# Kernel tuning notes

Hardware: AMD Instinct MI355X
Metric: run time of the kernel (lower is better)

Reference implementation:

```python
import jax, jax.numpy as jnp
import numpy as np

KCODES = 8  # kcodes from init


def setup_inputs() -> dict:
    key = jax.random.key(0)
    k1, k2 = jax.random.split(key)
    x = jax.random.normal(k1, (4, 2048, 768), dtype=jnp.float32)          # [B, S, D]
    codebook = jax.random.normal(k2, (8192, 768), dtype=jnp.float32)      # [N, D] embedding weight
    return {"x": x, "codebook": codebook}


def reference(x, codebook):
    # EuclideanSnapFunction.forward with default hook_kwargs
    # (keep_k_codes=True, no disabled codes/tokens):
    #   logits = -cdist(x, codebook, p=2); topk(kcodes); gather; mean over k.
    # Top-k over -dist is identical to top-k over -dist^2, so we use squared
    x2 = jnp.sum(x * x, axis=-1, keepdims=True)                 # [B, S, 1]
    c2 = jnp.sum(codebook * codebook, axis=-1)                  # [N]
    xc = jnp.einsum('bsd,nd->bsn', x, codebook)                 # [B, S, N]
    neg_d2 = 2.0 * xc - x2 - c2                                 # -squared dist
    _, codebook_ids = jax.lax.top_k(neg_d2, KCODES)             # [B, S, K]
    quant = codebook[codebook_ids]                              # [B, S, K, D] gather
    outputs = quant.sum(axis=-2) / KCODES                       # masked averaging over k codes
    return outputs, codebook_ids
```

## Files before the change

### kernel.cpp

```cpp
#include <hip/hip_runtime.h>

#define T_TOK 8192
#define DIM   768
#define NCB   8192
#define KSEL  8
#define BT    64
#define BN    128
#define BD    32
#define NQ    (BD/4)
#define CSTR  9
#define DSTR  140

typedef float v2f __attribute__((ext_vector_type(2)));

__global__ __launch_bounds__(256) void sq_pairwise_kernel(
    const float* __restrict__ cb, const float* __restrict__ x,
    float* __restrict__ c2out, float* __restrict__ x2out)
{
  #pragma clang fp contract(off)
  __shared__ float part[32][8];
  const int tid = threadIdx.x;
  const int row = blockIdx.x * 32 + (tid >> 3);
  const int b   = tid & 7;
  const float* src = (row < NCB) ? (cb + (size_t)row * DIM)
                                 : (x + (size_t)(row - NCB) * DIM);
  const float* a = src + 96 * b;

  float s[16];
  #pragma unroll
  for (int l = 0; l < 16; ++l) {
    float v, t;
    v = a[l];       t = v * v; float r0 = t;
    v = a[64 + l];  t = v * v; r0 = r0 + t;
    v = a[80 + l];  t = v * v; r0 = r0 + t;
    v = a[16 + l];  t = v * v; float r1 = t;
    v = a[32 + l];  t = v * v; float r2 = t;
    v = a[48 + l];  t = v * v; float r3 = t;
    s[l] = (r0 + r1) + (r2 + r3);
  }
  float t1[8], t2[4];
  #pragma unroll
  for (int i = 0; i < 8; ++i) t1[i] = s[i] + s[i + 8];
  #pragma unroll
  for (int j = 0; j < 4; ++j) t2[j] = t1[j] + t1[j + 4];
  part[tid >> 3][b] = (t2[0] + t2[2]) + (t2[1] + t2[3]);
  __syncthreads();

  if (b == 0) {
    const float* p = part[tid >> 3];
    float res = ((p[0] + p[1]) + (p[2] + p[3])) + ((p[4] + p[5]) + (p[6] + p[7]));
    if (row < NCB) c2out[row] = res;
    else           x2out[row - NCB] = res;
  }
}

__global__ __launch_bounds__(256, 2) void dist_topk_kernel(
    const float* __restrict__ x, const float* __restrict__ cb,
    const float* __restrict__ c2g, const float* __restrict__ x2g,
    float* __restrict__ ws, int ncodes)
{
  #pragma clang fp contract(off)
  __shared__ float4 smem4[2240];
  float*  smem = (float*)smem4;
  float4* xs4  = smem4;
  float4* cs4  = smem4 + NQ * BT;

  const int tid  = threadIdx.x;
  const int t0   = blockIdx.x * BT;
  const int nbeg = blockIdx.y * ncodes;

  const int gx = tid & 15;
  const int gy = tid >> 4;

  const int tt = tid >> 2;
  const int cc = tid & 3;

  const int xr  = tid >> 2;
  const int xq  = tid & 3;
  const int cr  = tid >> 1;
  const int cq0 = (tid & 1) * 4;
  const int crg = (cr >> 3) * CSTR + (cr & 7);

  float x2r[4];
  #pragma unroll
  for (int i = 0; i < 4; ++i) x2r[i] = x2g[t0 + gy * 4 + i];

  float bdist[KSEL]; int bid[KSEL];
  #pragma unroll
  for (int i = 0; i < KSEL; ++i) { bdist[i] = __builtin_inff(); bid[i] = 0x7fffffff; }
  float bmax = __builtin_inff(); int bmaxid = 0x7fffffff; int bslot = 0;

  for (int n0 = nbeg; n0 < nbeg + ncodes; n0 += BN) {
    float c2r[8];
    #pragma unroll
    for (int j = 0; j < 8; ++j) c2r[j] = c2g[n0 + gx * 8 + j];

    v2f accL[4][8], accH[4][8];
    #pragma unroll
    for (int i = 0; i < 4; ++i)
      #pragma unroll
      for (int j = 0; j < 8; ++j) { accL[i][j] = (v2f)0.f; accH[i][j] = (v2f)0.f; }

    float4 xpre0, xpre1, cpre0, cpre1, cpre2, cpre3;
    {
      const float* xp = x + (size_t)(t0 + xr) * DIM + xq * 4;
      xpre0 = *(const float4*)xp;
      xpre1 = *(const float4*)(xp + 16);
      const float* cp = cb + (size_t)(n0 + cr) * DIM + cq0 * 4;
      cpre0 = *(const float4*)(cp + 0);
      cpre1 = *(const float4*)(cp + 4);
      cpre2 = *(const float4*)(cp + 8);
      cpre3 = *(const float4*)(cp + 12);
    }

    for (int d0 = 0; d0 < DIM; d0 += BD) {
      __syncthreads();
      xs4[xq * BT + xr]       = xpre0;
      xs4[(xq + 4) * BT + xr] = xpre1;
      cs4[(cq0 + 0) * 16 * CSTR + crg] = cpre0;
      cs4[(cq0 + 1) * 16 * CSTR + crg] = cpre1;
      cs4[(cq0 + 2) * 16 * CSTR + crg] = cpre2;
      cs4[(cq0 + 3) * 16 * CSTR + crg] = cpre3;
      __syncthreads();

      const int dn = d0 + BD;
      if (dn < DIM) {
        const float* xp = x + (size_t)(t0 + xr) * DIM + dn + xq * 4;
        xpre0 = *(const float4*)xp;
        xpre1 = *(const float4*)(xp + 16);
        const float* cp = cb + (size_t)(n0 + cr) * DIM + dn + cq0 * 4;
        cpre0 = *(const float4*)(cp + 0);
        cpre1 = *(const float4*)(cp + 4);
        cpre2 = *(const float4*)(cp + 8);
        cpre3 = *(const float4*)(cp + 12);
      }

      #pragma unroll
      for (int q = 0; q < NQ; ++q) {
        float4 xa[4];
        #pragma unroll
        for (int i = 0; i < 4; ++i) xa[i] = xs4[q * BT + gy * 4 + i];
        #pragma unroll
        for (int j = 0; j < 8; ++j) {
          const float4 cv = cs4[q * 16 * CSTR + gx * CSTR + j];
          #pragma unroll
          for (int i = 0; i < 4; ++i) {
            v2f a, b, p;
            a[0] = xa[i].x; a[1] = xa[i].y;
            b[0] = cv.x;    b[1] = cv.y;
            p = a * b;
            accL[i][j] = accL[i][j] + p;
            a[0] = xa[i].z; a[1] = xa[i].w;
            b[0] = cv.z;    b[1] = cv.w;
            p = a * b;
            accH[i][j] = accH[i][j] + p;
          }
        }
      }
    }

    __syncthreads();
    #pragma unroll
    for (int i = 0; i < 4; ++i) {
      float v[8];
      #pragma unroll
      for (int j = 0; j < 8; ++j) {
        float xc = (accL[i][j][0] + accH[i][j][0]) + (accL[i][j][1] + accH[i][j][1]);
        float s  = 2.0f * xc - x2r[i];
        v[j] = -(s - c2r[j]);
      }
      float4* dp = (float4*)&smem[(gy * 4 + i) * DSTR + gx * 8];
      dp[0] = make_float4(v[0], v[1], v[2], v[3]);
      dp[1] = make_float4(v[4], v[5], v[6], v[7]);
    }
    __syncthreads();

    #pragma unroll
    for (int i2 = 0; i2 < BN / 4; ++i2) {
      const float dval = smem[tt * DSTR + cc + 4 * i2];
      const int   id   = n0 + cc + 4 * i2;
      if (dval < bmax) {
        #pragma unroll
        for (int q = 0; q < KSEL; ++q)
          if (q == bslot) { bdist[q] = dval; bid[q] = id; }
        bmax = bdist[0]; bmaxid = bid[0]; bslot = 0;
        #pragma unroll
        for (int q = 1; q < KSEL; ++q)
          if (bdist[q] > bmax || (bdist[q] == bmax && bid[q] > bmaxid)) {
            bmax = bdist[q]; bmaxid = bid[q]; bslot = q;
          }
      }
    }
  }

  __syncthreads();
  float* md = smem;
  int*   mi = (int*)smem + 2048;
  #pragma unroll
  for (int j = 0; j < KSEL; ++j) {
    md[tt * 32 + cc * KSEL + j] = bdist[j];
    mi[tt * 32 + cc * KSEL + j] = bid[j];
  }
  __syncthreads();
  if (tid < BT) {
    float* mdt = md + tid * 32;
    int*   mit = mi + tid * 32;
    const size_t base = ((size_t)blockIdx.y * T_TOK + (t0 + tid)) * 16;
    for (int r = 0; r < KSEL; ++r) {
      float best = __builtin_inff(); int bestid = 0x7fffffff; int bs = 0;
      for (int s = 0; s < 32; ++s) {
        const float dv = mdt[s]; const int iv = mit[s];
        if (dv < best || (dv == best && iv < bestid)) { best = dv; bestid = iv; bs = s; }
      }
      mdt[bs] = __builtin_inff();
      ws[base + r] = best;
      ((int*)ws)[base + 8 + r] = bestid;
    }
  }
}

__global__ __launch_bounds__(192) void merge_gather_kernel(
    const float* __restrict__ cb, const float* __restrict__ ws,
    float* __restrict__ out, float* __restrict__ out_ids, int nsplit)
{
  __shared__ float mv[64];
  __shared__ int   mid[64];
  __shared__ int   ssel[KSEL];

  const int t   = blockIdx.x;
  const int tid = threadIdx.x;
  const int ncand = nsplit * KSEL;

  if (tid < ncand) {
    const int s = tid >> 3, r = tid & 7;
    const size_t base = ((size_t)s * T_TOK + t) * 16;
    mv[tid]  = ws[base + r];
    mid[tid] = ((const int*)ws)[base + 8 + r];
  }
  __syncthreads();

  if (tid == 0) {
    for (int r = 0; r < KSEL; ++r) {
      float best = __builtin_inff(); int bestid = 0x7fffffff; int bs = 0;
      for (int s = 0; s < ncand; ++s) {
        const float dv = mv[s]; const int iv = mid[s];
        if (dv < best || (dv == best && iv < bestid)) { best = dv; bestid = iv; bs = s; }
      }
      mv[bs] = __builtin_inff();
      ssel[r] = bestid;
      out_ids[(size_t)t * KSEL + r] = (float)bestid;
    }
  }
  __syncthreads();

  float4 s4 = make_float4(0.f, 0.f, 0.f, 0.f);
  #pragma unroll
  for (int r = 0; r < KSEL; ++r) {
    const float4 v = *(const float4*)(cb + (size_t)ssel[r] * DIM + tid * 4);
    s4.x += v.x; s4.y += v.y; s4.z += v.z; s4.w += v.w;
  }
  s4.x *= 0.125f; s4.y *= 0.125f; s4.z *= 0.125f; s4.w *= 0.125f;
  *(float4*)(out + (size_t)t * DIM + tid * 4) = s4;
}

extern "C" void kernel_launch(void* const* d_in, const int* in_sizes, int n_in,
                              void* d_out, int out_size, void* d_ws, size_t ws_size,
                              hipStream_t stream) {
  (void)in_sizes; (void)n_in; (void)out_size;
  const float* x   = (const float*)d_in[0];
  const float* cbk = (const float*)d_in[1];
  float* out     = (float*)d_out;
  float* c2buf   = out;
  float* x2buf   = out + NCB;
  float* out_ids = out + (size_t)T_TOK * DIM;
  float* ws      = (float*)d_ws;

  int nsplit = 1;
  for (int s = 4; s >= 1; s >>= 1) {
    if ((size_t)s * T_TOK * 16 * 4 <= ws_size) { nsplit = s; break; }
  }
  const int ncodes = NCB / nsplit;

  sq_pairwise_kernel<<<(NCB + T_TOK) / 32, 256, 0, stream>>>(cbk, x, c2buf, x2buf);
  dist_topk_kernel<<<dim3(T_TOK / BT, nsplit), 256, 0, stream>>>(
      x, cbk, c2buf, x2buf, ws, ncodes);
  merge_gather_kernel<<<T_TOK, 192, 0, stream>>>(cbk, ws, out, out_ids, nsplit);
}
```

Measured before the change: 2.405 ms.

## Use direct global-to-LDS loads with double-buffered, XOR-swizzled shared tiles

```diff
diff --git a/kernel.cpp b/kernel.cpp
--- a/kernel.cpp
+++ b/kernel.cpp
@@ -8,10 +8,16 @@
 #define BN    128
 #define BD    32
 #define NQ    (BD/4)
-#define CSTR  9
 #define DSTR  140
+#define BUFQ  1536
 
 typedef float v2f __attribute__((ext_vector_type(2)));
+
+__device__ __forceinline__ void gload16(const float* g, float4* l) {
+  __builtin_amdgcn_global_load_lds(
+      (const __attribute__((address_space(1))) void*)g,
+      (__attribute__((address_space(3))) void*)l, 16, 0, 0);
+}
 
 __global__ __launch_bounds__(256) void sq_pairwise_kernel(
     const float* __restrict__ cb, const float* __restrict__ x,
@@ -60,10 +66,8 @@
     float* __restrict__ ws, int ncodes)
 {
   #pragma clang fp contract(off)
-  __shared__ float4 smem4[2240];
-  float*  smem = (float*)smem4;
-  float4* xs4  = smem4;
-  float4* cs4  = smem4 + NQ * BT;
+  __shared__ float4 smem4[2 * BUFQ];
+  float* smem = (float*)smem4;
 
   const int tid  = threadIdx.x;
   const int t0   = blockIdx.x * BT;
@@ -71,15 +75,25 @@
 
   const int gx = tid & 15;
   const int gy = tid >> 4;
+  const int g7 = gx & 7;
 
   const int tt = tid >> 2;
   const int cc = tid & 3;
 
-  const int xr  = tid >> 2;
-  const int xq  = tid & 3;
-  const int cr  = tid >> 1;
-  const int cq0 = (tid & 1) * 4;
-  const int crg = (cr >> 3) * CSTR + (cr & 7);
+  const int lane = tid & 63;
+  const int wid  = tid >> 6;
+
+  const float* xsrcA = x + (size_t)(t0 + lane) * DIM + wid * 4;
+  const float* xsrcB = xsrcA + 16;
+
+  const int s0_ = 0 * 256 + wid * 64 + lane;
+  const int s1_ = 1 * 256 + wid * 64 + lane;
+  const int s2_ = 2 * 256 + wid * 64 + lane;
+  const int s3_ = 3 * 256 + wid * 64 + lane;
+  const int c0_ = s0_ >> 3, q0_ = (s0_ & 7) ^ ((s0_ >> 6) & 7);
+  const int c1_ = s1_ >> 3, q1_ = (s1_ & 7) ^ ((s1_ >> 6) & 7);
+  const int c2_ = s2_ >> 3, q2_ = (s2_ & 7) ^ ((s2_ >> 6) & 7);
+  const int c3_ = s3_ >> 3, q3_ = (s3_ & 7) ^ ((s3_ >> 6) & 7);
 
   float x2r[4];
   #pragma unroll
@@ -101,48 +115,50 @@
       #pragma unroll
       for (int j = 0; j < 8; ++j) { accL[i][j] = (v2f)0.f; accH[i][j] = (v2f)0.f; }
 
-    float4 xpre0, xpre1, cpre0, cpre1, cpre2, cpre3;
+    const float* csrc0 = cb + (size_t)(n0 + c0_) * DIM + q0_ * 4;
+    const float* csrc1 = cb + (size_t)(n0 + c1_) * DIM + q1_ * 4;
+    const float* csrc2 = cb + (size_t)(n0 + c2_) * DIM + q2_ * 4;
+    const float* csrc3 = cb + (size_t)(n0 + c3_) * DIM + q3_ * 4;
+
+    __syncthreads();
     {
-      const float* xp = x + (size_t)(t0 + xr) * DIM + xq * 4;
-      xpre0 = *(const float4*)xp;
-      xpre1 = *(const float4*)(xp + 16);
-      const float* cp = cb + (size_t)(n0 + cr) * DIM + cq0 * 4;
-      cpre0 = *(const float4*)(cp + 0);
-      cpre1 = *(const float4*)(cp + 4);
-      cpre2 = *(const float4*)(cp + 8);
-      cpre3 = *(const float4*)(cp + 12);
-    }
+      float4* xsn = smem4;
+      float4* csn = smem4 + 512;
+      gload16(xsrcA, xsn + wid * 64);
+      gload16(xsrcB, xsn + 256 + wid * 64);
+      gload16(csrc0, csn + 0   + wid * 64);
+      gload16(csrc1, csn + 256 + wid * 64);
+      gload16(csrc2, csn + 512 + wid * 64);
+      gload16(csrc3, csn + 768 + wid * 64);
+    }
+    __syncthreads();
 
     for (int d0 = 0; d0 < DIM; d0 += BD) {
-      __syncthreads();
-      xs4[xq * BT + xr]       = xpre0;
-      xs4[(xq + 4) * BT + xr] = xpre1;
-      cs4[(cq0 + 0) * 16 * CSTR + crg] = cpre0;
-      cs4[(cq0 + 1) * 16 * CSTR + crg] = cpre1;
-      cs4[(cq0 + 2) * 16 * CSTR + crg] = cpre2;
-      cs4[(cq0 + 3) * 16 * CSTR + crg] = cpre3;
-      __syncthreads();
+      const int buf = (d0 >> 5) & 1;
+      const float4* xsb = smem4 + buf * BUFQ;
+      const float4* csb = xsb + 512;
 
       const int dn = d0 + BD;
       if (dn < DIM) {
-        const float* xp = x + (size_t)(t0 + xr) * DIM + dn + xq * 4;
-        xpre0 = *(const float4*)xp;
-        xpre1 = *(const float4*)(xp + 16);
-        const float* cp = cb + (size_t)(n0 + cr) * DIM + dn + cq0 * 4;
-        cpre0 = *(const float4*)(cp + 0);
-        cpre1 = *(const float4*)(cp + 4);
-        cpre2 = *(const float4*)(cp + 8);
-        cpre3 = *(const float4*)(cp + 12);
+        float4* xsn = smem4 + (buf ^ 1) * BUFQ;
+        float4* csn = xsn + 512;
+        gload16(xsrcA + dn, xsn + wid * 64);
+        gload16(xsrcB + dn, xsn + 256 + wid * 64);
+        gload16(csrc0 + dn, csn + 0   + wid * 64);
+        gload16(csrc1 + dn, csn + 256 + wid * 64);
+        gload16(csrc2 + dn, csn + 512 + wid * 64);
+        gload16(csrc3 + dn, csn + 768 + wid * 64);
       }
 
       #pragma unroll
       for (int q = 0; q < NQ; ++q) {
         float4 xa[4];
         #pragma unroll
-        for (int i = 0; i < 4; ++i) xa[i] = xs4[q * BT + gy * 4 + i];
+        for (int i = 0; i < 4; ++i) xa[i] = xsb[q * BT + gy * 4 + i];
+        const float4* cq = csb + gx * 64 + (q ^ g7);
         #pragma unroll
         for (int j = 0; j < 8; ++j) {
-          const float4 cv = cs4[q * 16 * CSTR + gx * CSTR + j];
+          const float4 cv = cq[j * 8];
           #pragma unroll
           for (int i = 0; i < 4; ++i) {
             v2f a, b, p;
@@ -157,9 +173,9 @@
           }
         }
       }
-    }
-
-    __syncthreads();
+      __syncthreads();
+    }
+
     #pragma unroll
     for (int i = 0; i < 4; ++i) {
       float v[8];
```

After: 2.430 ms. Within noise of the previous version (+1.0%).
